# Optimization experiments

Measured on AMD Instinct MI355X. Metric: run time of the kernel, lower is better.

The kernel has to match this reference:

```python
import jax, jax.numpy as jnp
import numpy as np

O, I, B, H, W = 128, 128, 32, 112, 112
STRIDE, PAD = 1, 1

def _synth_weight(core, periphery, threshold, scale):
    # core: (O,I,1,1); periphery: (8,); threshold: (O,); scale: (1,)
    c = core[:, :, 0, 0]                                   # (O,I) center tap
    # threshold-gated scale: soft gate on periphery contribution per (o,i)
    gate = jax.nn.sigmoid(scale[0] * (jnp.abs(c) - threshold[:, None]))  # (O,I)
    # 9 flattened taps: index 4 is center (weight 1), others use shared periphery
    p_full = jnp.concatenate([periphery[:4], jnp.ones((1,), c.dtype), periphery[4:]])  # (9,)
    is_center = (jnp.arange(9) == 4).astype(c.dtype)        # (9,)
    gate_k = is_center[None, None, :] + (1.0 - is_center)[None, None, :] * gate[:, :, None]
    w = c[:, :, None] * p_full[None, None, :] * gate_k      # (O,I,9)
    return w.reshape(c.shape[0], c.shape[1], 3, 3)          # (O,I,3,3)

def setup_inputs() -> dict:
    key = jax.random.key(0)
    kx, kc, kp = jax.random.split(key, 3)
    x = jax.random.normal(kx, (B, I, H, W), dtype=jnp.float32)
    # kaiming-uniform-ish core init
    bound = float(np.sqrt(6.0 / I))
    core = jax.random.uniform(kc, (O, I, 1, 1), minval=-bound, maxval=bound, dtype=jnp.float32)
    periphery = jax.random.uniform(kp, (8,), minval=-0.1, maxval=0.1, dtype=jnp.float32)
    threshold = jnp.full((O,), 0.1, dtype=jnp.float32)
    scale = jnp.array([10.0], dtype=jnp.float32)
    return {"x": x, "core": core, "periphery": periphery, "threshold": threshold, "scale": scale}

def reference(x, core, periphery, threshold, scale):
    w = _synth_weight(core, periphery, threshold, scale)    # (O,I,3,3)
    return jax.lax.conv_general_dilated(
        x, w,
        window_strides=(STRIDE, STRIDE),
        padding=[(PAD, PAD), (PAD, PAD)],
        dimension_numbers=("NCHW", "OIHW", "NCHW"),
    )
```

## Files before the change

kernel.cpp:

```cpp
#include <hip/hip_runtime.h>

typedef short short8 __attribute__((ext_vector_type(8)));
typedef float f32x4 __attribute__((ext_vector_type(4)));
typedef unsigned short ushort8_t __attribute__((ext_vector_type(8)));

#define O_CH 128
#define I_CH 128
#define HW 112
#define PLANE (HW * HW)
#define NCOL 114
#define BUFB (3 * NCOL * 64)

__device__ __forceinline__ unsigned short f2bf(float f) {
  union { float f; unsigned u; } v; v.f = f;
  unsigned r = v.u + 0x7FFFu + ((v.u >> 16) & 1u);
  return (unsigned short)(r >> 16);
}

__device__ __forceinline__ unsigned pktrunc(float lo, float hi) {
  union { float f; unsigned u; } a, b; a.f = lo; b.f = hi;
  return __builtin_amdgcn_perm(b.u, a.u, 0x07060302u);
}

__global__ void wsynth_kernel(const float* __restrict__ core,
                              const float* __restrict__ periph,
                              const float* __restrict__ thr,
                              const float* __restrict__ scale,
                              unsigned short* __restrict__ Wb) {
  int idx = blockIdx.x * blockDim.x + threadIdx.x;
  if (idx >= O_CH * I_CH) return;
  int o = idx >> 7;
  float c = core[idx];
  float s = scale[0];
  float g = 1.0f / (1.0f + __expf(-s * (fabsf(c) - thr[o])));
#pragma unroll
  for (int tap = 0; tap < 9; ++tap) {
    float p  = (tap == 4) ? 1.0f : periph[tap < 4 ? tap : tap - 1];
    float gg = (tap == 4) ? 1.0f : g;
    Wb[tap * (O_CH * I_CH) + idx] = f2bf(c * p * gg);
  }
}

__global__ __launch_bounds__(256, 3)
void conv_kernel(const float* __restrict__ X,
                 const unsigned short* __restrict__ Wb,
                 float* __restrict__ Out) {
  __shared__ unsigned short Xs[2 * 3 * NCOL * 32];
  char* lds = (char*)Xs;

  const int bid = blockIdx.x;
  const int L = (bid & 7) * 448 + (bid >> 3);
  const int b = L / HW;
  const int y = L - b * HW;

  const int t   = threadIdx.x;
  const int wv  = t >> 6;
  const int l   = t & 63;
  const int ln  = l & 15;
  const int lk4 = l >> 4;

  const int c    = t & 127;
  const int chb  = (t >> 7) * 16;
  const int icol = c - 1;
  const bool cok = (c < NCOL);
  const int wxor = (c >> 1) & 3;

  f32x4 acc[2][7];
#pragma unroll
  for (int mr = 0; mr < 2; ++mr)
#pragma unroll
    for (int nf = 0; nf < 7; ++nf)
      acc[mr][nf] = (f32x4)0.0f;

  const unsigned short* wbase = Wb + (wv * 32 + ln) * I_CH + lk4 * 8;

#define LOAD16(V, KCH, SUB)                                                     \
  {                                                                             \
    const int row_ = y + (SUB)-1;                                               \
    const bool ok_ = (row_ >= 0) && (row_ < HW) && (icol >= 0) && (icol < HW);  \
    const float* sp_ = X + ((size_t)(b * I_CH + (KCH) + chb) * HW + row_) * HW  \
                       + icol;                                                  \
    _Pragma("unroll") for (int j = 0; j < 16; ++j) V[j] = 0.0f;                 \
    if (ok_) {                                                                  \
      _Pragma("unroll") for (int j = 0; j < 16; ++j) V[j] = sp_[j * PLANE];     \
    }                                                                           \
  }

#define WRITE16(V, SUB, WB)                                                     \
  if (cok) {                                                                    \
    const int base_ = ((SUB)*NCOL + c) * 64;                                    \
    _Pragma("unroll") for (int q = 0; q < 2; ++q) {                             \
      union { ushort8_t s; unsigned u[4]; } pk_;                                \
      pk_.u[0] = pktrunc(V[q * 8 + 0], V[q * 8 + 1]);                           \
      pk_.u[1] = pktrunc(V[q * 8 + 2], V[q * 8 + 3]);                           \
      pk_.u[2] = pktrunc(V[q * 8 + 4], V[q * 8 + 5]);                           \
      pk_.u[3] = pktrunc(V[q * 8 + 6], V[q * 8 + 7]);                           \
      const int slot_ = ((chb >> 3) + q) ^ wxor;                                \
      *reinterpret_cast<ushort8_t*>((WB) + base_ + slot_ * 16) = pk_.s;         \
    }                                                                           \
  }

#define APFETCH(D0, D1, Q)                                                      \
  _Pragma("unroll") for (int dx = 0; dx < 3; ++dx) {                            \
    const unsigned short* wp_ = wbase + (((Q) % 3) * 3 + dx) * (O_CH * I_CH)    \
                              + ((Q) / 3) * 32;                                 \
    D0[dx] = *reinterpret_cast<const short8*>(wp_);                             \
    D1[dx] = *reinterpret_cast<const short8*>(wp_ + 16 * I_CH);                 \
  }

#define COMPUTE_SUB_REG(SUB, RB, S0, S1)                                        \
  _Pragma("unroll") for (int dx = 0; dx < 3; ++dx) {                            \
    const int q_ = dx + ln;                                                     \
    const int rslot_ = lk4 ^ ((q_ >> 1) & 3);      \
    const char* bp_ = (RB) + ((SUB)*NCOL + q_) * 64 + rslot_ * 16;              \
    _Pragma("unroll") for (int nf = 0; nf < 7; ++nf) {                          \
      short8 bb_ = *reinterpret_cast<const short8*>(bp_ + nf * 1024);           \
      acc[0][nf] = __builtin_amdgcn_mfma_f32_16x16x32_bf16(S0[dx], bb_, acc[0][nf], 0, 0, 0); \
      acc[1][nf] = __builtin_amdgcn_mfma_f32_16x16x32_bf16(S1[dx], bb_, acc[1][nf], 0, 0, 0); \
    }                                                                           \
  }

  short8 A0[3], A1[3], N0[3], N1[3];

  {
    float P0[16], P1[16], P2[16];
    LOAD16(P0, 0, 0)
    LOAD16(P1, 0, 1)
    LOAD16(P2, 0, 2)
    APFETCH(A0, A1, 0)
    WRITE16(P0, 0, lds)
    WRITE16(P1, 1, lds)
    WRITE16(P2, 2, lds)
  }
  __syncthreads();

#pragma unroll
  for (int k = 0; k < 4; ++k) {
    char* rbuf = lds + (k & 1) * BUFB;
    char* wbuf = lds + ((k & 1) ^ 1) * BUFB;
    float LA[16], LB[16];
    const int q0 = k * 3;

    if (k < 3) LOAD16(LA, (k + 1) * 32, 0)
    APFETCH(N0, N1, q0 + 1)
    COMPUTE_SUB_REG(0, rbuf, A0, A1)
#pragma unroll
    for (int dx = 0; dx < 3; ++dx) { A0[dx] = N0[dx]; A1[dx] = N1[dx]; }

    if (k < 3) LOAD16(LB, (k + 1) * 32, 1)
    APFETCH(N0, N1, q0 + 2)
    COMPUTE_SUB_REG(1, rbuf, A0, A1)
    if (k < 3) WRITE16(LA, 0, wbuf)
#pragma unroll
    for (int dx = 0; dx < 3; ++dx) { A0[dx] = N0[dx]; A1[dx] = N1[dx]; }

    if (k < 3) LOAD16(LA, (k + 1) * 32, 2)
    if (k < 3) APFETCH(N0, N1, q0 + 3)
    COMPUTE_SUB_REG(2, rbuf, A0, A1)
    if (k < 3) {
      WRITE16(LB, 1, wbuf)
      WRITE16(LA, 2, wbuf)
#pragma unroll
      for (int dx = 0; dx < 3; ++dx) { A0[dx] = N0[dx]; A1[dx] = N1[dx]; }
      __syncthreads();
    }
  }

  const int obase = wv * 32 + lk4 * 4;
  float* outp = Out + (size_t)b * O_CH * PLANE + (size_t)y * HW;
#pragma unroll
  for (int mr = 0; mr < 2; ++mr) {
#pragma unroll
    for (int j = 0; j < 4; ++j) {
      const int o = obase + mr * 16 + j;
      float* po = outp + (size_t)o * PLANE;
#pragma unroll
      for (int nf = 0; nf < 7; ++nf) {
        po[nf * 16 + ln] = acc[mr][nf][j];
      }
    }
  }
}

extern "C" void kernel_launch(void* const* d_in, const int* in_sizes, int n_in,
                              void* d_out, int out_size, void* d_ws, size_t ws_size,
                              hipStream_t stream) {
  const float* x      = (const float*)d_in[0];
  const float* core   = (const float*)d_in[1];
  const float* periph = (const float*)d_in[2];
  const float* thr    = (const float*)d_in[3];
  const float* scale  = (const float*)d_in[4];
  unsigned short* Wb  = (unsigned short*)d_ws;

  wsynth_kernel<<<(O_CH * I_CH + 255) / 256, 256, 0, stream>>>(core, periph, thr, scale, Wb);

  const int grid = 32 * HW;
  conv_kernel<<<grid, 256, 0, stream>>>(x, Wb, (float*)d_out);
}
```

Measured before the change: 204.8 us.

## Pre-pack input to padded bf16 NHWC and stage tiles via global_load_lds DMA

Adds a prep kernel that converts the fp32 NCHW input into a zero-padded bf16 channels-last buffer in workspace. The conv kernel then loads its input tiles straight into LDS with global_load_lds, using a zero-filled region for out-of-bounds rows, so the per-block fp32 loads, bf16 packing and swizzled LDS writes go away. This cuts register pressure and VALU work inside the conv loop, but adds an extra pass that writes and rereads the whole input. The old path is kept as a fallback when the workspace is too small.

```diff
diff --git a/kernel.cpp b/kernel.cpp
--- a/kernel.cpp
+++ b/kernel.cpp
@@ -3,13 +3,18 @@
 typedef short short8 __attribute__((ext_vector_type(8)));
 typedef float f32x4 __attribute__((ext_vector_type(4)));
 typedef unsigned short ushort8_t __attribute__((ext_vector_type(8)));
+typedef const __attribute__((address_space(1))) void gvoid_t;
+typedef __attribute__((address_space(3))) void lvoid_t;
 
 #define O_CH 128
 #define I_CH 128
 #define HW 112
 #define PLANE (HW * HW)
 #define NCOL 114
-#define BUFB (3 * NCOL * 64)
+#define XPCOLS 128
+#define WB_OFF   8192
+#define XP_OFF   303104
+#define WS_NEED  117743616ULL
 
 __device__ __forceinline__ unsigned short f2bf(float f) {
   union { float f; unsigned u; } v; v.f = f;
@@ -41,12 +46,56 @@
   }
 }
 
+__global__ void zfill_kernel(float* ws) {
+  float4* p = (float4*)ws;
+  p[threadIdx.x * 2]     = make_float4(0.f, 0.f, 0.f, 0.f);
+  p[threadIdx.x * 2 + 1] = make_float4(0.f, 0.f, 0.f, 0.f);
+}
+
+__global__ __launch_bounds__(256) void xprep_kernel(const float* __restrict__ X,
+                                                    unsigned short* __restrict__ Xp) {
+  __shared__ float T[128 * 65];
+  const int wg = blockIdx.x;
+  const int b = wg / 224;
+  const int rem = wg - b * 224;
+  const int y = rem >> 1;
+  const int cb = (rem & 1) * 64;
+
+  const int t = threadIdx.x;
+  const int chq = t >> 2, part = t & 3;
+#pragma unroll
+  for (int i = 0; i < 2; ++i) {
+    const int ch = i * 64 + chq;
+    const float* xr = X + ((size_t)(b * I_CH + ch) * HW + y) * HW;
+#pragma unroll
+    for (int j = 0; j < 16; ++j) {
+      const int c  = cb + part * 16 + j;
+      const int ic = c - 1;
+      T[ch * 65 + part * 16 + j] = (ic >= 0 && ic < HW) ? xr[ic] : 0.0f;
+    }
+  }
+  __syncthreads();
+
+  const int col = t & 63, chh = t >> 6;
+  const int c = cb + col;
+  unsigned u[16];
+#pragma unroll
+  for (int q = 0; q < 16; ++q) {
+    u[q] = pktrunc(T[(chh * 32 + 2 * q) * 65 + col],
+                   T[(chh * 32 + 2 * q + 1) * 65 + col]);
+  }
+  uint4* dst = (uint4*)(Xp + ((size_t)(b * HW + y) * XPCOLS + c) * 128 + chh * 32);
+#pragma unroll
+  for (int q = 0; q < 4; ++q)
+    dst[q] = make_uint4(u[q * 4], u[q * 4 + 1], u[q * 4 + 2], u[q * 4 + 3]);
+}
+
 __global__ __launch_bounds__(256, 3)
-void conv_kernel(const float* __restrict__ X,
-                 const unsigned short* __restrict__ Wb,
-                 float* __restrict__ Out) {
-  __shared__ unsigned short Xs[2 * 3 * NCOL * 32];
-  char* lds = (char*)Xs;
+void conv_dma(const unsigned short* __restrict__ Xp,
+              const unsigned short* __restrict__ Wb,
+              const char* __restrict__ zbase,
+              float* __restrict__ Out) {
+  __shared__ unsigned short Xs[2 * 3 * XPCOLS * 32];
 
   const int bid = blockIdx.x;
   const int L = (bid & 7) * 448 + (bid >> 3);
@@ -59,6 +108,119 @@
   const int ln  = l & 15;
   const int lk4 = l >> 4;
 
+  f32x4 acc[2][7];
+#pragma unroll
+  for (int mr = 0; mr < 2; ++mr)
+#pragma unroll
+    for (int nf = 0; nf < 7; ++nf)
+      acc[mr][nf] = (f32x4)0.0f;
+
+  const unsigned short* wbase = Wb + (wv * 32 + ln) * I_CH + lk4 * 8;
+  char* lds0 = (char*)Xs;
+
+#define STAGE_DMA(K, BUF)                                                       \
+  _Pragma("unroll") for (int j = 0; j < 6; ++j) {                               \
+    const int lin_  = j * 256 + t;                                              \
+    const int row_  = lin_ >> 9;                                                \
+    const int rem_  = lin_ & 511;                                               \
+    const int irow_ = y - 1 + row_;                                             \
+    const char* src_ = (irow_ >= 0 && irow_ < HW)                               \
+        ? (const char*)Xp + ((size_t)(b * HW + irow_) * XPCOLS + (rem_ >> 2)) * 256 \
+              + (K) * 64 + (rem_ & 3) * 16                                      \
+        : zbase + rem_ * 16;                                                    \
+    void* dst_ = (char*)(BUF) + j * 4096 + (t >> 6) * 1024;                     \
+    __builtin_amdgcn_global_load_lds((gvoid_t*)src_, (lvoid_t*)dst_, 16, 0, 0); \
+  }
+
+#define APFETCH(D0, D1, Q)                                                      \
+  _Pragma("unroll") for (int dx = 0; dx < 3; ++dx) {                            \
+    const unsigned short* wp_ = wbase + (((Q) % 3) * 3 + dx) * (O_CH * I_CH)    \
+                              + ((Q) / 3) * 32;                                 \
+    D0[dx] = *reinterpret_cast<const short8*>(wp_);                             \
+    D1[dx] = *reinterpret_cast<const short8*>(wp_ + 16 * I_CH);                 \
+  }
+
+#define COMPUTE_SUB_DMA(SUB, RB, S0, S1)                                        \
+  _Pragma("unroll") for (int dx = 0; dx < 3; ++dx) {                            \
+    const char* bp_ = (RB) + (SUB) * 8192 + (dx + ln) * 64 + lk4 * 16;          \
+    _Pragma("unroll") for (int nf = 0; nf < 7; ++nf) {                          \
+      short8 bb_ = *reinterpret_cast<const short8*>(bp_ + nf * 1024);           \
+      acc[0][nf] = __builtin_amdgcn_mfma_f32_16x16x32_bf16(S0[dx], bb_, acc[0][nf], 0, 0, 0); \
+      acc[1][nf] = __builtin_amdgcn_mfma_f32_16x16x32_bf16(S1[dx], bb_, acc[1][nf], 0, 0, 0); \
+    }                                                                           \
+  }
+
+  short8 A0[3], A1[3], N0[3], N1[3];
+
+  APFETCH(A0, A1, 0)
+  STAGE_DMA(0, lds0)
+  __syncthreads();
+
+#pragma unroll
+  for (int k = 0; k < 4; ++k) {
+    char* rbuf = lds0 + (k & 1) * 24576;
+    char* wbuf = lds0 + ((k & 1) ^ 1) * 24576;
+    const int q0 = k * 3;
+
+    APFETCH(N0, N1, q0 + 1)
+    if (k < 3) STAGE_DMA(k + 1, wbuf)
+    COMPUTE_SUB_DMA(0, rbuf, A0, A1)
+#pragma unroll
+    for (int dx = 0; dx < 3; ++dx) { A0[dx] = N0[dx]; A1[dx] = N1[dx]; }
+
+    APFETCH(N0, N1, q0 + 2)
+    COMPUTE_SUB_DMA(1, rbuf, A0, A1)
+#pragma unroll
+    for (int dx = 0; dx < 3; ++dx) { A0[dx] = N0[dx]; A1[dx] = N1[dx]; }
+
+    if (k < 3) APFETCH(N0, N1, q0 + 3)
+    COMPUTE_SUB_DMA(2, rbuf, A0, A1)
+    if (k < 3) {
+#pragma unroll
+      for (int dx = 0; dx < 3; ++dx) { A0[dx] = N0[dx]; A1[dx] = N1[dx]; }
+      __syncthreads();
+    }
+  }
+
+  const int obase = wv * 32 + lk4 * 4;
+  float* outp = Out + (size_t)b * O_CH * PLANE + (size_t)y * HW;
+#pragma unroll
+  for (int mr = 0; mr < 2; ++mr) {
+#pragma unroll
+    for (int j = 0; j < 4; ++j) {
+      const int o = obase + mr * 16 + j;
+      float* po = outp + (size_t)o * PLANE;
+#pragma unroll
+      for (int nf = 0; nf < 7; ++nf) {
+        po[nf * 16 + ln] = acc[mr][nf][j];
+      }
+    }
+  }
+#undef STAGE_DMA
+#undef APFETCH
+#undef COMPUTE_SUB_DMA
+}
+
+#define BUFB_F (3 * NCOL * 64)
+
+__global__ __launch_bounds__(256, 3)
+void conv_r9(const float* __restrict__ X,
+             const unsigned short* __restrict__ Wb,
+             float* __restrict__ Out) {
+  __shared__ unsigned short Xs[2 * 3 * NCOL * 32];
+  char* lds = (char*)Xs;
+
+  const int bid = blockIdx.x;
+  const int L = (bid & 7) * 448 + (bid >> 3);
+  const int b = L / HW;
+  const int y = L - b * HW;
+
+  const int t   = threadIdx.x;
+  const int wv  = t >> 6;
+  const int l   = t & 63;
+  const int ln  = l & 15;
+  const int lk4 = l >> 4;
+
   const int c    = t & 127;
   const int chb  = (t >> 7) * 16;
   const int icol = c - 1;
@@ -74,7 +236,7 @@
 
   const unsigned short* wbase = Wb + (wv * 32 + ln) * I_CH + lk4 * 8;
 
-#define LOAD16(V, KCH, SUB)                                                     \
+#define LOAD16_F(V, KCH, SUB)                                                   \
   {                                                                             \
     const int row_ = y + (SUB)-1;                                               \
     const bool ok_ = (row_ >= 0) && (row_ < HW) && (icol >= 0) && (icol < HW);  \
@@ -86,7 +248,7 @@
     }                                                                           \
   }
 
-#define WRITE16(V, SUB, WB)                                                     \
+#define WRITE16_F(V, SUB, WB)                                                   \
   if (cok) {                                                                    \
     const int base_ = ((SUB)*NCOL + c) * 64;                                    \
     _Pragma("unroll") for (int q = 0; q < 2; ++q) {                             \
@@ -100,7 +262,7 @@
     }                                                                           \
   }
 
-#define APFETCH(D0, D1, Q)                                                      \
+#define APFETCH_F(D0, D1, Q)                                                    \
   _Pragma("unroll") for (int dx = 0; dx < 3; ++dx) {                            \
     const unsigned short* wp_ = wbase + (((Q) % 3) * 3 + dx) * (O_CH * I_CH)    \
                               + ((Q) / 3) * 32;                                 \
@@ -108,10 +270,10 @@
     D1[dx] = *reinterpret_cast<const short8*>(wp_ + 16 * I_CH);                 \
   }
 
-#define COMPUTE_SUB_REG(SUB, RB, S0, S1)                                        \
+#define COMPUTE_F(SUB, RB, S0, S1)                                              \
   _Pragma("unroll") for (int dx = 0; dx < 3; ++dx) {                            \
     const int q_ = dx + ln;                                                     \
-    const int rslot_ = lk4 ^ ((q_ >> 1) & 3);      \
+    const int rslot_ = lk4 ^ ((q_ >> 1) & 3);                                   \
     const char* bp_ = (RB) + ((SUB)*NCOL + q_) * 64 + rslot_ * 16;              \
     _Pragma("unroll") for (int nf = 0; nf < 7; ++nf) {                          \
       short8 bb_ = *reinterpret_cast<const short8*>(bp_ + nf * 1024);           \
@@ -121,45 +283,44 @@
   }
 
   short8 A0[3], A1[3], N0[3], N1[3];
-
   {
     float P0[16], P1[16], P2[16];
-    LOAD16(P0, 0, 0)
-    LOAD16(P1, 0, 1)
-    LOAD16(P2, 0, 2)
-    APFETCH(A0, A1, 0)
-    WRITE16(P0, 0, lds)
-    WRITE16(P1, 1, lds)
-    WRITE16(P2, 2, lds)
+    LOAD16_F(P0, 0, 0)
+    LOAD16_F(P1, 0, 1)
+    LOAD16_F(P2, 0, 2)
+    APFETCH_F(A0, A1, 0)
+    WRITE16_F(P0, 0, lds)
+    WRITE16_F(P1, 1, lds)
+    WRITE16_F(P2, 2, lds)
   }
   __syncthreads();
 
 #pragma unroll
   for (int k = 0; k < 4; ++k) {
-    char* rbuf = lds + (k & 1) * BUFB;
-    char* wbuf = lds + ((k & 1) ^ 1) * BUFB;
+    char* rbuf = lds + (k & 1) * BUFB_F;
+    char* wbuf = lds + ((k & 1) ^ 1) * BUFB_F;
     float LA[16], LB[16];
     const int q0 = k * 3;
 
-    if (k < 3) LOAD16(LA, (k + 1) * 32, 0)
-    APFETCH(N0, N1, q0 + 1)
-    COMPUTE_SUB_REG(0, rbuf, A0, A1)
+    if (k < 3) LOAD16_F(LA, (k + 1) * 32, 0)
+    APFETCH_F(N0, N1, q0 + 1)
+    COMPUTE_F(0, rbuf, A0, A1)
 #pragma unroll
     for (int dx = 0; dx < 3; ++dx) { A0[dx] = N0[dx]; A1[dx] = N1[dx]; }
 
-    if (k < 3) LOAD16(LB, (k + 1) * 32, 1)
-    APFETCH(N0, N1, q0 + 2)
-    COMPUTE_SUB_REG(1, rbuf, A0, A1)
-    if (k < 3) WRITE16(LA, 0, wbuf)
+    if (k < 3) LOAD16_F(LB, (k + 1) * 32, 1)
+    APFETCH_F(N0, N1, q0 + 2)
+    COMPUTE_F(1, rbuf, A0, A1)
+    if (k < 3) WRITE16_F(LA, 0, wbuf)
 #pragma unroll
     for (int dx = 0; dx < 3; ++dx) { A0[dx] = N0[dx]; A1[dx] = N1[dx]; }
 
-    if (k < 3) LOAD16(LA, (k + 1) * 32, 2)
-    if (k < 3) APFETCH(N0, N1, q0 + 3)
-    COMPUTE_SUB_REG(2, rbuf, A0, A1)
+    if (k < 3) LOAD16_F(LA, (k + 1) * 32, 2)
+    if (k < 3) APFETCH_F(N0, N1, q0 + 3)
+    COMPUTE_F(2, rbuf, A0, A1)
     if (k < 3) {
-      WRITE16(LB, 1, wbuf)
-      WRITE16(LA, 2, wbuf)
+      WRITE16_F(LB, 1, wbuf)
+      WRITE16_F(LA, 2, wbuf)
 #pragma unroll
       for (int dx = 0; dx < 3; ++dx) { A0[dx] = N0[dx]; A1[dx] = N1[dx]; }
       __syncthreads();
@@ -190,10 +351,17 @@
   const float* periph = (const float*)d_in[2];
   const float* thr    = (const float*)d_in[3];
   const float* scale  = (const float*)d_in[4];
-  unsigned short* Wb  = (unsigned short*)d_ws;
-
-  wsynth_kernel<<<(O_CH * I_CH + 255) / 256, 256, 0, stream>>>(core, periph, thr, scale, Wb);
-
-  const int grid = 32 * HW;
-  conv_kernel<<<grid, 256, 0, stream>>>(x, Wb, (float*)d_out);
-}
+
+  if (ws_size >= WS_NEED) {
+    unsigned short* Wb = (unsigned short*)((char*)d_ws + WB_OFF);
+    unsigned short* Xp = (unsigned short*)((char*)d_ws + XP_OFF);
+    wsynth_kernel<<<(O_CH * I_CH + 255) / 256, 256, 0, stream>>>(core, periph, thr, scale, Wb);
+    zfill_kernel<<<1, 256, 0, stream>>>((float*)d_ws);
+    xprep_kernel<<<32 * HW * 2, 256, 0, stream>>>(x, Xp);
+    conv_dma<<<32 * HW, 256, 0, stream>>>(Xp, Wb, (const char*)d_ws, (float*)d_out);
+  } else {
+    unsigned short* Wb = (unsigned short*)d_ws;
+    wsynth_kernel<<<(O_CH * I_CH + 255) / 256, 256, 0, stream>>>(core, periph, thr, scale, Wb);
+    conv_r9<<<32 * HW, 256, 0, stream>>>(x, Wb, (float*)d_out);
+  }
+}
```

After: 435.5 us. 113% more time.

## Compute two output rows per block to reuse input rows and weights

Applied to the files above, without the earlier changes.

Each block now produces two adjacent output rows instead of one. It stages four input rows per channel chunk in LDS, shared across both rows, and reuses each weight fragment for both row accumulators. This cuts the redundant global input reads (four rows loaded per two outputs instead of three per one) and halves the weight fetches per output, and the grid is halved to match. In exchange it doubles the accumulator registers, enlarges LDS, and drops the occupancy hint from launch bounds, so fewer waves may be resident.

```diff
diff --git a/kernel.cpp b/kernel.cpp
--- a/kernel.cpp
+++ b/kernel.cpp
@@ -9,7 +9,7 @@
 #define HW 112
 #define PLANE (HW * HW)
 #define NCOL 114
-#define BUFB (3 * NCOL * 64)
+#define BUFB (4 * NCOL * 64)
 
 __device__ __forceinline__ unsigned short f2bf(float f) {
   union { float f; unsigned u; } v; v.f = f;
@@ -41,17 +41,18 @@
   }
 }
 
-__global__ __launch_bounds__(256, 3)
+__global__ __launch_bounds__(256)
 void conv_kernel(const float* __restrict__ X,
                  const unsigned short* __restrict__ Wb,
                  float* __restrict__ Out) {
-  __shared__ unsigned short Xs[2 * 3 * NCOL * 32];
+  __shared__ unsigned short Xs[2 * 4 * NCOL * 32];
   char* lds = (char*)Xs;
 
   const int bid = blockIdx.x;
-  const int L = (bid & 7) * 448 + (bid >> 3);
-  const int b = L / HW;
-  const int y = L - b * HW;
+  const int L = (bid & 7) * 224 + (bid >> 3);
+  const int b = L / 56;
+  const int yp = L - b * 56;
+  const int y0 = yp * 2;
 
   const int t   = threadIdx.x;
   const int wv  = t >> 6;
@@ -65,18 +66,20 @@
   const bool cok = (c < NCOL);
   const int wxor = (c >> 1) & 3;
 
-  f32x4 acc[2][7];
-#pragma unroll
-  for (int mr = 0; mr < 2; ++mr)
-#pragma unroll
-    for (int nf = 0; nf < 7; ++nf)
-      acc[mr][nf] = (f32x4)0.0f;
+  f32x4 acc[2][2][7];
+#pragma unroll
+  for (int r = 0; r < 2; ++r)
+#pragma unroll
+    for (int mr = 0; mr < 2; ++mr)
+#pragma unroll
+      for (int nf = 0; nf < 7; ++nf)
+        acc[r][mr][nf] = (f32x4)0.0f;
 
   const unsigned short* wbase = Wb + (wv * 32 + ln) * I_CH + lk4 * 8;
 
-#define LOAD16(V, KCH, SUB)                                                     \
+#define LOAD16(V, KCH, S)                                                       \
   {                                                                             \
-    const int row_ = y + (SUB)-1;                                               \
+    const int row_ = y0 + (S)-1;                                                \
     const bool ok_ = (row_ >= 0) && (row_ < HW) && (icol >= 0) && (icol < HW);  \
     const float* sp_ = X + ((size_t)(b * I_CH + (KCH) + chb) * HW + row_) * HW  \
                        + icol;                                                  \
@@ -86,9 +89,9 @@
     }                                                                           \
   }
 
-#define WRITE16(V, SUB, WB)                                                     \
+#define WRITE16(V, S, WB)                                                       \
   if (cok) {                                                                    \
-    const int base_ = ((SUB)*NCOL + c) * 64;                                    \
+    const int base_ = ((S)*NCOL + c) * 64;                                      \
     _Pragma("unroll") for (int q = 0; q < 2; ++q) {                             \
       union { ushort8_t s; unsigned u[4]; } pk_;                                \
       pk_.u[0] = pktrunc(V[q * 8 + 0], V[q * 8 + 1]);                           \
@@ -100,37 +103,41 @@
     }                                                                           \
   }
 
-#define APFETCH(D0, D1, Q)                                                      \
+#define APF(AF, TAPB, K)                                                        \
   _Pragma("unroll") for (int dx = 0; dx < 3; ++dx) {                            \
-    const unsigned short* wp_ = wbase + (((Q) % 3) * 3 + dx) * (O_CH * I_CH)    \
-                              + ((Q) / 3) * 32;                                 \
-    D0[dx] = *reinterpret_cast<const short8*>(wp_);                             \
-    D1[dx] = *reinterpret_cast<const short8*>(wp_ + 16 * I_CH);                 \
-  }
-
-#define COMPUTE_SUB_REG(SUB, RB, S0, S1)                                        \
+    const unsigned short* wp_ = wbase + ((TAPB) + dx) * (O_CH * I_CH) + (K)*32; \
+    AF[dx][0] = *reinterpret_cast<const short8*>(wp_);                          \
+    AF[dx][1] = *reinterpret_cast<const short8*>(wp_ + 16 * I_CH);              \
+  }
+
+#define COMPUTE_S(S, RB, A0F, A1F, USE0, USE1)                                  \
   _Pragma("unroll") for (int dx = 0; dx < 3; ++dx) {                            \
     const int q_ = dx + ln;                                                     \
     const int rslot_ = lk4 ^ ((q_ >> 1) & 3);      \
-    const char* bp_ = (RB) + ((SUB)*NCOL + q_) * 64 + rslot_ * 16;              \
+    const char* bp_ = (RB) + ((S)*NCOL + q_) * 64 + rslot_ * 16;                \
     _Pragma("unroll") for (int nf = 0; nf < 7; ++nf) {                          \
       short8 bb_ = *reinterpret_cast<const short8*>(bp_ + nf * 1024);           \
-      acc[0][nf] = __builtin_amdgcn_mfma_f32_16x16x32_bf16(S0[dx], bb_, acc[0][nf], 0, 0, 0); \
-      acc[1][nf] = __builtin_amdgcn_mfma_f32_16x16x32_bf16(S1[dx], bb_, acc[1][nf], 0, 0, 0); \
+      if (USE0) {                                                               \
+        acc[0][0][nf] = __builtin_amdgcn_mfma_f32_16x16x32_bf16(A0F[dx][0], bb_, acc[0][0][nf], 0, 0, 0); \
+        acc[0][1][nf] = __builtin_amdgcn_mfma_f32_16x16x32_bf16(A0F[dx][1], bb_, acc[0][1][nf], 0, 0, 0); \
+      }                                                                         \
+      if (USE1) {                                                               \
+        acc[1][0][nf] = __builtin_amdgcn_mfma_f32_16x16x32_bf16(A1F[dx][0], bb_, acc[1][0][nf], 0, 0, 0); \
+        acc[1][1][nf] = __builtin_amdgcn_mfma_f32_16x16x32_bf16(A1F[dx][1], bb_, acc[1][1][nf], 0, 0, 0); \
+      }                                                                         \
     }                                                                           \
   }
 
-  short8 A0[3], A1[3], N0[3], N1[3];
-
   {
-    float P0[16], P1[16], P2[16];
+    float P0[16], P1[16];
     LOAD16(P0, 0, 0)
     LOAD16(P1, 0, 1)
-    LOAD16(P2, 0, 2)
-    APFETCH(A0, A1, 0)
     WRITE16(P0, 0, lds)
     WRITE16(P1, 1, lds)
-    WRITE16(P2, 2, lds)
+    LOAD16(P0, 0, 2)
+    LOAD16(P1, 0, 3)
+    WRITE16(P0, 2, lds)
+    WRITE16(P1, 3, lds)
   }
   __syncthreads();
 
@@ -139,44 +146,48 @@
     char* rbuf = lds + (k & 1) * BUFB;
     char* wbuf = lds + ((k & 1) ^ 1) * BUFB;
     float LA[16], LB[16];
-    const int q0 = k * 3;
-
+    short8 AF0[3][2], AF1[3][2];
+
+    APF(AF0, 0, k)
     if (k < 3) LOAD16(LA, (k + 1) * 32, 0)
-    APFETCH(N0, N1, q0 + 1)
-    COMPUTE_SUB_REG(0, rbuf, A0, A1)
-#pragma unroll
-    for (int dx = 0; dx < 3; ++dx) { A0[dx] = N0[dx]; A1[dx] = N1[dx]; }
-
+    COMPUTE_S(0, rbuf, AF0, AF1, 1, 0)
+
+    APF(AF0, 3, k)
+    APF(AF1, 0, k)
     if (k < 3) LOAD16(LB, (k + 1) * 32, 1)
-    APFETCH(N0, N1, q0 + 2)
-    COMPUTE_SUB_REG(1, rbuf, A0, A1)
+    COMPUTE_S(1, rbuf, AF0, AF1, 1, 1)
     if (k < 3) WRITE16(LA, 0, wbuf)
-#pragma unroll
-    for (int dx = 0; dx < 3; ++dx) { A0[dx] = N0[dx]; A1[dx] = N1[dx]; }
-
+
+    APF(AF0, 6, k)
+    APF(AF1, 3, k)
     if (k < 3) LOAD16(LA, (k + 1) * 32, 2)
-    if (k < 3) APFETCH(N0, N1, q0 + 3)
-    COMPUTE_SUB_REG(2, rbuf, A0, A1)
+    COMPUTE_S(2, rbuf, AF0, AF1, 1, 1)
+    if (k < 3) WRITE16(LB, 1, wbuf)
+
+    APF(AF1, 6, k)
+    if (k < 3) LOAD16(LB, (k + 1) * 32, 3)
+    COMPUTE_S(3, rbuf, AF0, AF1, 0, 1)
     if (k < 3) {
-      WRITE16(LB, 1, wbuf)
       WRITE16(LA, 2, wbuf)
-#pragma unroll
-      for (int dx = 0; dx < 3; ++dx) { A0[dx] = N0[dx]; A1[dx] = N1[dx]; }
+      WRITE16(LB, 3, wbuf)
       __syncthreads();
     }
   }
 
   const int obase = wv * 32 + lk4 * 4;
-  float* outp = Out + (size_t)b * O_CH * PLANE + (size_t)y * HW;
-#pragma unroll
-  for (int mr = 0; mr < 2; ++mr) {
-#pragma unroll
-    for (int j = 0; j < 4; ++j) {
-      const int o = obase + mr * 16 + j;
-      float* po = outp + (size_t)o * PLANE;
-#pragma unroll
-      for (int nf = 0; nf < 7; ++nf) {
-        po[nf * 16 + ln] = acc[mr][nf][j];
+#pragma unroll
+  for (int r = 0; r < 2; ++r) {
+    float* outp = Out + (size_t)b * O_CH * PLANE + (size_t)(y0 + r) * HW;
+#pragma unroll
+    for (int mr = 0; mr < 2; ++mr) {
+#pragma unroll
+      for (int j = 0; j < 4; ++j) {
+        const int o = obase + mr * 16 + j;
+        float* po = outp + (size_t)o * PLANE;
+#pragma unroll
+        for (int nf = 0; nf < 7; ++nf) {
+          po[nf * 16 + ln] = acc[r][mr][nf][j];
+        }
       }
     }
   }
@@ -194,6 +205,6 @@
 
   wsynth_kernel<<<(O_CH * I_CH + 255) / 256, 256, 0, stream>>>(core, periph, thr, scale, Wb);
 
-  const int grid = 32 * HW;
+  const int grid = 32 * (HW / 2);
   conv_kernel<<<grid, 256, 0, stream>>>(x, Wb, (float*)d_out);
 }
```

Measured after the change: 224.3 us. 1.1x slower.
